# Performance work log

Hardware: AMD Instinct MI355X
Metric: run time of the kernel (lower is better)

## Reference

```python
import jax, jax.numpy as jnp
import numpy as np

B, N0, N1, N2, HS, NCLS = 16384, 57, 20, 10, 5, 17
EPS = 1e-4  # SPDRectified eigenvalue floor
_TRI = np.triu_indices(HS)  # upper-tri vectorization indices


def _bilinear(x, W):
    # SPDTransform: W^T X W, W: (in, out) column-orthonormal (Stiefel)
    return jnp.einsum('ji,bjk,kl->bil', W, x, W)


def _rectify(x):
    # SPDRectified: eigh, clamp eigenvalues at EPS, recompose
    w, v = jnp.linalg.eigh(x)
    w = jnp.maximum(w, EPS)
    return jnp.einsum('bij,bj,bkj->bik', v, w, v)


def _logmap(x):
    # SPDTangentSpace log map: eigh, log eigenvalues, recompose
    w, v = jnp.linalg.eigh(x)
    w = jnp.log(w)
    return jnp.einsum('bij,bj,bkj->bik', v, w, v)


def setup_inputs() -> dict:
    key = jax.random.key(0)
    ks = jax.random.split(key, 6)
    A = jax.random.normal(ks[0], (B, N0, N0), dtype=jnp.float32)
    # SPD input: A A^T / N0 + 0.01 I
    x = jnp.einsum('bij,bkj->bik', A, A) / N0 + 0.01 * jnp.eye(N0, dtype=jnp.float32)

    def stiefel(k, m, n):
        q, _ = jnp.linalg.qr(jax.random.normal(k, (m, n), dtype=jnp.float32))
        return q  # (m, n) column-orthonormal

    W1 = stiefel(ks[1], N0, N1)
    W2 = stiefel(ks[2], N1, N2)
    W3 = stiefel(ks[3], N2, HS)
    tri = HS * (HS + 1) // 2
    lin_w = jax.random.normal(ks[4], (NCLS, tri), dtype=jnp.float32) / np.sqrt(tri)
    lin_b = jax.random.normal(ks[5], (NCLS,), dtype=jnp.float32) * 0.01
    return {"x": x, "W1": W1, "W2": W2, "W3": W3, "lin_w": lin_w, "lin_b": lin_b}


def reference(x, W1, W2, W3, lin_w, lin_b):
    x = _rectify(_bilinear(x, W1))   # [B,20,20]
    x = _rectify(_bilinear(x, W2))   # [B,10,10]
    x = _rectify(_bilinear(x, W3))   # [B,HS,HS]
    x = _logmap(x)                   # tangent space
    vec = x[:, _TRI[0], _TRI[1]]     # [B, HS*(HS+1)/2]
    return vec @ lin_w.T + lin_b     # [B, 17]
```

## Files before the change

### kernel.cpp

```cpp
#include <hip/hip_runtime.h>
#include <math.h>

#define BATCH 16384
#define N0 57
#define NX 3249
#define GPB 4
#define HS 5
#define NCLS 17
#define NTRI 15
#define EPSV 1e-4f

template<int CTRL>
__device__ __forceinline__ float dpp_mov0(float x) {
    return __int_as_float(__builtin_amdgcn_update_dpp(
        0, __float_as_int(x), CTRL, 0xF, 0xF, true));
}
__device__ __forceinline__ float wave_sum64(float x) {
    x += dpp_mov0<0x111>(x);
    x += dpp_mov0<0x112>(x);
    x += dpp_mov0<0x114>(x);
    x += dpp_mov0<0x118>(x);
    x += dpp_mov0<0x142>(x);
    x += dpp_mov0<0x143>(x);
    return x;
}

__device__ __forceinline__ void load_lds16(const float* g, float* l) {
    __builtin_amdgcn_global_load_lds(
        (const __attribute__((address_space(1))) void*)g,
        (__attribute__((address_space(3))) void*)l, 16, 0, 0);
}

__global__ __launch_bounds__(128) void k_setup(const float* __restrict__ W1,
                                               const float* __restrict__ W2,
                                               const float* __restrict__ W3,
                                               float* __restrict__ wc_out) {
    __shared__ float w23[100];
    int t = threadIdx.x;
    if (t < 100) {
        int k = t / 5, j = t % 5;
        float acc = 0.f;
        for (int l = 0; l < 10; ++l) acc = fmaf(W2[k * 10 + l], W3[l * 5 + j], acc);
        w23[t] = acc;
    }
    __syncthreads();
    if (t < N0) {
        float r[5];
        #pragma unroll
        for (int j = 0; j < 5; ++j) {
            float acc = 0.f;
            for (int k = 0; k < 20; ++k) acc = fmaf(W1[t * 20 + k], w23[k * 5 + j], acc);
            r[j] = acc;
        }
        float4* o = (float4*)&wc_out[t * 8];
        o[0] = make_float4(r[0], r[1], r[2], r[3]);
        o[1] = make_float4(r[4], 0.f, 0.f, 0.f);
    }
}

__global__ __launch_bounds__(256) void k_main(const float* __restrict__ x,
                                              const float* __restrict__ wc,
                                              float* __restrict__ y_out) {
    __shared__ float xs[13312];
    const int tid  = threadIdx.x;
    const int lane = tid & 63;
    const int wave = tid >> 6;

    float wv[HS];
    {
        int a = (lane < N0) ? lane : 0;
        const float4* wp = (const float4*)&wc[a * 8];
        float4 v0 = wp[0];
        float  v4 = wc[a * 8 + 4];
        wv[0] = v0.x; wv[1] = v0.y; wv[2] = v0.z; wv[3] = v0.w; wv[4] = v4;
        if (lane >= N0) { wv[0] = wv[1] = wv[2] = wv[3] = wv[4] = 0.f; }
    }

    const float* gbase = x + (size_t)blockIdx.x * (GPB * NX);
    #pragma unroll
    for (int r = 0; r < 13; ++r) {
        int slot = r * 256 + tid;
        int cs = slot > 3248 ? 3248 : slot;
        load_lds16(gbase + (size_t)cs * 4, &xs[r * 1024 + (tid & 192) * 4]);
    }

    asm volatile("s_waitcnt vmcnt(0)" ::: "memory");
    __builtin_amdgcn_s_barrier();

    const float* base = &xs[wave * NX];
    float s[HS] = {0.f, 0.f, 0.f, 0.f, 0.f};
    #pragma unroll
    for (int b = 0; b < N0; ++b) {
        float xv = base[b * N0 + lane];
        #pragma unroll
        for (int j = 0; j < HS; ++j) s[j] = fmaf(xv, wc[b * 8 + j], s[j]);
    }

    float p[NTRI];
    int t = 0;
    #pragma unroll
    for (int i = 0; i < HS; ++i)
        #pragma unroll
        for (int j = i; j < HS; ++j) { p[t] = wave_sum64(wv[i] * s[j]); ++t; }

    if (lane == 63) {
        float4* o = (float4*)&y_out[(size_t)(blockIdx.x * GPB + wave) * 16];
        o[0] = make_float4(p[0],  p[1],  p[2],  p[3]);
        o[1] = make_float4(p[4],  p[5],  p[6],  p[7]);
        o[2] = make_float4(p[8],  p[9],  p[10], p[11]);
        o[3] = make_float4(p[12], p[13], p[14], 0.f);
    }
}

__global__ __launch_bounds__(64) void k_eig(const float* __restrict__ y_in,
                                            const float* __restrict__ lin_w,
                                            const float* __restrict__ lin_b,
                                            float* __restrict__ out) {
    __shared__ float lws[NCLS * NTRI];
    __shared__ float lbs[NCLS];
    int tid = threadIdx.x;
    for (int i = tid; i < NCLS * NTRI; i += 64) lws[i] = lin_w[i];
    if (tid < NCLS) lbs[tid] = lin_b[tid];
    __syncthreads();

    int m = blockIdx.x * 64 + tid;
    const float4* yin = (const float4*)&y_in[(size_t)m * 16];
    float4 q0 = yin[0], q1 = yin[1], q2 = yin[2], q3 = yin[3];
    float tri[16] = {q0.x, q0.y, q0.z, q0.w, q1.x, q1.y, q1.z, q1.w,
                     q2.x, q2.y, q2.z, q2.w, q3.x, q3.y, q3.z, q3.w};

    float A[HS][HS], V[HS][HS];
    int t = 0;
    #pragma unroll
    for (int i = 0; i < HS; ++i)
        #pragma unroll
        for (int j = i; j < HS; ++j) { A[i][j] = tri[t]; A[j][i] = tri[t]; ++t; }
    #pragma unroll
    for (int i = 0; i < HS; ++i)
        #pragma unroll
        for (int j = 0; j < HS; ++j) V[i][j] = (i == j) ? 1.f : 0.f;

    #pragma unroll
    for (int sweep = 0; sweep < 6; ++sweep) {
        #pragma unroll
        for (int p = 0; p < HS - 1; ++p) {
            #pragma unroll
            for (int q = p + 1; q < HS; ++q) {
                float apq = A[p][q];
                float app = A[p][p], aqq = A[q][q];
                bool nz = fabsf(apq) > 1e-30f;
                float denom = nz ? 2.f * apq : 1.f;
                float tau = (aqq - app) / denom;
                float tt = 1.f / (fabsf(tau) + sqrtf(fmaf(tau, tau, 1.f)));
                tt = copysignf(tt, tau);
                tt = nz ? tt : 0.f;
                float c = rsqrtf(fmaf(tt, tt, 1.f));
                float sn = tt * c;
                #pragma unroll
                for (int k = 0; k < HS; ++k) {
                    float akp = A[k][p], akq = A[k][q];
                    A[k][p] = fmaf(c, akp, -sn * akq);
                    A[k][q] = fmaf(sn, akp,  c * akq);
                }
                #pragma unroll
                for (int k = 0; k < HS; ++k) {
                    float apk = A[p][k], aqk = A[q][k];
                    A[p][k] = fmaf(c, apk, -sn * aqk);
                    A[q][k] = fmaf(sn, apk,  c * aqk);
                }
                #pragma unroll
                for (int k = 0; k < HS; ++k) {
                    float vkp = V[k][p], vkq = V[k][q];
                    V[k][p] = fmaf(c, vkp, -sn * vkq);
                    V[k][q] = fmaf(sn, vkp,  c * vkq);
                }
            }
        }
    }

    float lwv[HS];
    #pragma unroll
    for (int i = 0; i < HS; ++i) lwv[i] = logf(fmaxf(A[i][i], EPSV));

    float tri2[NTRI];
    t = 0;
    #pragma unroll
    for (int i = 0; i < HS; ++i) {
        float vi[HS];
        #pragma unroll
        for (int k = 0; k < HS; ++k) vi[k] = V[i][k] * lwv[k];
        #pragma unroll
        for (int j = i; j < HS; ++j) {
            float acc = 0.f;
            #pragma unroll
            for (int k = 0; k < HS; ++k) acc = fmaf(vi[k], V[j][k], acc);
            tri2[t++] = acc;
        }
    }

    #pragma unroll
    for (int c = 0; c < NCLS; ++c) {
        float acc = lbs[c];
        #pragma unroll
        for (int k = 0; k < NTRI; ++k) acc = fmaf(tri2[k], lws[c * NTRI + k], acc);
        out[(size_t)m * NCLS + c] = acc;
    }
}

extern "C" void kernel_launch(void* const* d_in, const int* in_sizes, int n_in,
                              void* d_out, int out_size, void* d_ws, size_t ws_size,
                              hipStream_t stream) {
    const float* x     = (const float*)d_in[0];
    const float* W1    = (const float*)d_in[1];
    const float* W2    = (const float*)d_in[2];
    const float* W3    = (const float*)d_in[3];
    const float* lin_w = (const float*)d_in[4];
    const float* lin_b = (const float*)d_in[5];
    float* out = (float*)d_out;
    float* ws  = (float*)d_ws;
    float* wc  = ws;
    float* y   = ws + 512;

    k_setup<<<1, 128, 0, stream>>>(W1, W2, W3, wc);
    k_main<<<BATCH / GPB, 256, 0, stream>>>(x, wc, y);
    k_eig<<<BATCH / 64, 64, 0, stream>>>(y, lin_w, lin_b, out);
}
```

Baseline: 58.35 us.

## Double-buffer LDS tiles in a persistent main kernel looping over sixteen tiles

The main kernel now launches sixteen times fewer blocks, and each block walks sixteen consecutive four-matrix tiles. Two LDS buffers let the asynchronous global-to-LDS load of the next tile run while the current tile is reduced, with a partial vmcnt wait and barriers between steps. The aim is to hide load latency and cut per-block launch and setup overhead. The cost is double the LDS per block (about 104KB), which allows only one block and four waves per CU. That leaves fewer bytes in flight than the earlier setup of several resident blocks per CU.

```diff
diff --git a/kernel.cpp b/kernel.cpp
--- a/kernel.cpp
+++ b/kernel.cpp
@@ -9,6 +9,8 @@
 #define NCLS 17
 #define NTRI 15
 #define EPSV 1e-4f
+#define NT 16
+#define BUFF 13312
 
 template<int CTRL>
 __device__ __forceinline__ float dpp_mov0(float x) {
@@ -29,6 +31,15 @@
     __builtin_amdgcn_global_load_lds(
         (const __attribute__((address_space(1))) void*)g,
         (__attribute__((address_space(3))) void*)l, 16, 0, 0);
+}
+
+__device__ __forceinline__ void stage_tile(const float* gbase, float* buf, int tid) {
+    #pragma unroll
+    for (int r = 0; r < 13; ++r) {
+        int slot = r * 256 + tid;
+        int cs = slot > 3248 ? 3248 : slot;
+        load_lds16(gbase + (size_t)cs * 4, &buf[r * 1024 + (tid & 192) * 4]);
+    }
 }
 
 __global__ __launch_bounds__(128) void k_setup(const float* __restrict__ W1,
@@ -61,7 +72,7 @@
 __global__ __launch_bounds__(256) void k_main(const float* __restrict__ x,
                                               const float* __restrict__ wc,
                                               float* __restrict__ y_out) {
-    __shared__ float xs[13312];
+    __shared__ float xs[2 * BUFF];
     const int tid  = threadIdx.x;
     const int lane = tid & 63;
     const int wave = tid >> 6;
@@ -76,39 +87,46 @@
         if (lane >= N0) { wv[0] = wv[1] = wv[2] = wv[3] = wv[4] = 0.f; }
     }
 
-    const float* gbase = x + (size_t)blockIdx.x * (GPB * NX);
-    #pragma unroll
-    for (int r = 0; r < 13; ++r) {
-        int slot = r * 256 + tid;
-        int cs = slot > 3248 ? 3248 : slot;
-        load_lds16(gbase + (size_t)cs * 4, &xs[r * 1024 + (tid & 192) * 4]);
-    }
-
-    asm volatile("s_waitcnt vmcnt(0)" ::: "memory");
-    __builtin_amdgcn_s_barrier();
-
-    const float* base = &xs[wave * NX];
-    float s[HS] = {0.f, 0.f, 0.f, 0.f, 0.f};
-    #pragma unroll
-    for (int b = 0; b < N0; ++b) {
-        float xv = base[b * N0 + lane];
-        #pragma unroll
-        for (int j = 0; j < HS; ++j) s[j] = fmaf(xv, wc[b * 8 + j], s[j]);
-    }
-
-    float p[NTRI];
-    int t = 0;
-    #pragma unroll
-    for (int i = 0; i < HS; ++i)
-        #pragma unroll
-        for (int j = i; j < HS; ++j) { p[t] = wave_sum64(wv[i] * s[j]); ++t; }
-
-    if (lane == 63) {
-        float4* o = (float4*)&y_out[(size_t)(blockIdx.x * GPB + wave) * 16];
-        o[0] = make_float4(p[0],  p[1],  p[2],  p[3]);
-        o[1] = make_float4(p[4],  p[5],  p[6],  p[7]);
-        o[2] = make_float4(p[8],  p[9],  p[10], p[11]);
-        o[3] = make_float4(p[12], p[13], p[14], 0.f);
+    const size_t tile0 = (size_t)blockIdx.x * NT;
+
+    stage_tile(x + tile0 * (GPB * NX), xs, tid);
+
+    for (int t = 0; t < NT; ++t) {
+        float* cur = xs + (t & 1) * BUFF;
+        float* nxt = xs + ((t + 1) & 1) * BUFF;
+
+        if (t + 1 < NT) {
+            stage_tile(x + (tile0 + t + 1) * (GPB * NX), nxt, tid);
+            asm volatile("s_waitcnt vmcnt(13)" ::: "memory");
+        } else {
+            asm volatile("s_waitcnt vmcnt(0)" ::: "memory");
+        }
+        __builtin_amdgcn_s_barrier();
+
+        const float* base = cur + wave * NX;
+        float s[HS] = {0.f, 0.f, 0.f, 0.f, 0.f};
+        #pragma unroll
+        for (int b = 0; b < N0; ++b) {
+            float xv = base[b * N0 + lane];
+            #pragma unroll
+            for (int j = 0; j < HS; ++j) s[j] = fmaf(xv, wc[b * 8 + j], s[j]);
+        }
+
+        float p[NTRI];
+        int u = 0;
+        #pragma unroll
+        for (int i = 0; i < HS; ++i)
+            #pragma unroll
+            for (int j = i; j < HS; ++j) { p[u] = wave_sum64(wv[i] * s[j]); ++u; }
+
+        if (lane == 63) {
+            float4* o = (float4*)&y_out[(size_t)((tile0 + t) * GPB + wave) * 16];
+            o[0] = make_float4(p[0],  p[1],  p[2],  p[3]);
+            o[1] = make_float4(p[4],  p[5],  p[6],  p[7]);
+            o[2] = make_float4(p[8],  p[9],  p[10], p[11]);
+            o[3] = make_float4(p[12], p[13], p[14], 0.f);
+        }
+        __builtin_amdgcn_s_barrier();
     }
 }
 
@@ -222,6 +240,6 @@
     float* y   = ws + 512;
 
     k_setup<<<1, 128, 0, stream>>>(W1, W2, W3, wc);
-    k_main<<<BATCH / GPB, 256, 0, stream>>>(x, wc, y);
+    k_main<<<BATCH / (GPB * NT), 256, 0, stream>>>(x, wc, y);
     k_eig<<<BATCH / 64, 64, 0, stream>>>(y, lin_w, lin_b, out);
 }
```

New measurement: 66.13 us. 13.3% more time.
